# Optimization experiments

Measured on AMD Instinct MI355X. Metric: run time of the kernel, lower is better.

The kernel has to match this reference:

```python
import jax, jax.numpy as jnp
import numpy as np

B, D = 65536, 365

def _linp(k, fan_in, fan_out):
    # torch nn.Linear default init: U(-1/sqrt(fan_in), 1/sqrt(fan_in))
    kw, kb = jax.random.split(k)
    bound = 1.0 / np.sqrt(fan_in)
    W = jax.random.uniform(kw, (fan_in, fan_out), jnp.float32, -bound, bound)
    b = jax.random.uniform(kb, (fan_out,), jnp.float32, -bound, bound)
    return W, b

def setup_inputs() -> dict:
    key = jax.random.key(0)
    ks = jax.random.split(key, 9)
    x = jax.random.normal(ks[0], (B, D), jnp.float32)
    W1, b1 = _linp(ks[1], D, 512)
    W2, b2 = _linp(ks[2], 512, 256)
    W3, b3 = _linp(ks[3], 256, 128)
    Ws, bs = _linp(ks[4], 6, 32)
    Wc1, bc1 = _linp(ks[5], 128 + 32, 64)
    Wc2, bc2 = _linp(ks[6], 64, 32)
    Wc3, bc3 = _linp(ks[7], 32, 1)
    return dict(x=x, W1=W1, b1=b1, W2=W2, b2=b2, W3=W3, b3=b3,
                Ws=Ws, bs=bs, Wc1=Wc1, bc1=bc1, Wc2=Wc2, bc2=bc2,
                Wc3=Wc3, bc3=bc3)

def _row_stats(x):
    # fused row-wise moments: mean, std (ddof=1), min, max, skew, kurtosis
    mu = jnp.mean(x, axis=1, keepdims=True)          # [B,1]
    c = x - mu                                        # [B,D]
    var1 = jnp.sum(c * c, axis=1) / (x.shape[1] - 1)  # unbiased, matches torch.std()
    sigma = jnp.sqrt(var1)
    m3 = jnp.mean(c ** 3, axis=1)
    m4 = jnp.mean(c ** 4, axis=1)
    skew = m3 / (sigma ** 3 + 1e-8)
    kurt = m4 / (sigma ** 4 + 1e-8)
    return jnp.stack([mu[:, 0], sigma, jnp.min(x, axis=1), jnp.max(x, axis=1), skew, kurt], axis=1)

def reference(x, W1, b1, W2, b2, W3, b3, Ws, bs, Wc1, bc1, Wc2, bc2, Wc3, bc3):
    h = jax.nn.relu(x @ W1 + b1)
    h = jax.nn.relu(h @ W2 + b2)
    seq = jax.nn.relu(h @ W3 + b3)            # [B,128]
    stat = _row_stats(x) @ Ws + bs            # [B,32]
    comb = jnp.concatenate([seq, stat], axis=1)
    c = jax.nn.relu(comb @ Wc1 + bc1)
    c = jax.nn.relu(c @ Wc2 + bc2)
    out = jax.nn.sigmoid(c @ Wc3 + bc3)       # [B,1]
    return out[:, 0]
```

## Files before the change

### kernel.cpp

```cpp
#include <hip/hip_runtime.h>
#include <math.h>

typedef __attribute__((ext_vector_type(8)))  short short8;
typedef __attribute__((ext_vector_type(16))) float float16;
typedef __attribute__((ext_vector_type(4), aligned(4))) float float4a;

#define DEVI __device__ __forceinline__

DEVI short f2bf(float f) {
    unsigned u = __float_as_uint(f);
    u = (u + 0x7fffu + ((u >> 16) & 1u)) >> 16;
    return (short)u;
}
DEVI unsigned pk2(float a, float b) {
    return (unsigned)(unsigned short)f2bf(a) | ((unsigned)(unsigned short)f2bf(b) << 16);
}
DEVI float16 mfma16(short8 a, short8 b, float16 c) {
    return __builtin_amdgcn_mfma_f32_32x32x16_bf16(a, b, c, 0, 0, 0);
}
DEVI int rowof(int r, int h) { return (r & 3) + 8 * (r >> 2) + 4 * h; }
DEVI short8 lds8(const short* p) { return *(const short8*)p; }
DEVI short8 gld8(const short* p) { return *(const short8*)p; }

#define W1T_OFF  0
#define W2T_OFF  188416
#define W3T_OFF  319488
#define WC1T_OFF 352256
#define WC2T_OFF 362496

__global__ void prep_v2(const float* __restrict__ W1, const float* __restrict__ W2,
                        const float* __restrict__ W3, const float* __restrict__ Wc1,
                        const float* __restrict__ Wc2, short* __restrict__ ws) {
    __shared__ short T[16 * 72];
    int b = blockIdx.x, t = threadIdx.x;
    const float* src; int K, N; size_t base; int kc, nb;
    if (b < 184)        {            src = W1;  K = 365; N = 512; base = W1T_OFF;  kc = b >> 3;  nb = b & 7; }
    else if (b < 312)   { int l = b - 184; src = W2;  K = 512; N = 256; base = W2T_OFF;  kc = l >> 2;  nb = l & 3; }
    else if (b < 344)   { int l = b - 312; src = W3;  K = 256; N = 128; base = W3T_OFF;  kc = l >> 1;  nb = l & 1; }
    else if (b < 354)   {            src = Wc1; K = 160; N = 64;  base = WC1T_OFF; kc = b - 344; nb = 0; }
    else                {            src = Wc2; K = 64;  N = 32;  base = WC2T_OFF; kc = b - 354; nb = 0; }
    int n = nb * 64 + (t & 63);
    int kr = t >> 6;
    #pragma unroll
    for (int i = 0; i < 4; ++i) {
        int krow = kr + 4 * i;
        int k = kc * 16 + krow;
        float v = (k < K && n < N) ? src[(size_t)k * N + n] : 0.f;
        T[krow * 72 + (t & 63)] = f2bf(v);
    }
    __syncthreads();
    int n2 = t >> 2, ksq = (t & 3) * 4;
    int ng = nb * 64 + n2;
    if (ng < N) {
        unsigned lo = (unsigned)(unsigned short)T[ksq * 72 + n2]
                    | ((unsigned)(unsigned short)T[(ksq + 1) * 72 + n2] << 16);
        unsigned hi = (unsigned)(unsigned short)T[(ksq + 2) * 72 + n2]
                    | ((unsigned)(unsigned short)T[(ksq + 3) * 72 + n2] << 16);
        uint2 d; d.x = lo; d.y = hi;
        *(uint2*)(ws + base + ((size_t)kc * N + ng) * 16 + ksq) = d;
    }
}

__global__ __launch_bounds__(512, 4)
void fused_v7(const float* __restrict__ x,
              const float* __restrict__ b1f, const float* __restrict__ b2f,
              const float* __restrict__ b3f, const float* __restrict__ Wsf,
              const float* __restrict__ bsf, const float* __restrict__ bc1f,
              const float* __restrict__ bc2f, const float* __restrict__ Wc3f,
              const float* __restrict__ bc3f,
              const short* __restrict__ wsw, float* __restrict__ out)
{
    __shared__ __align__(16) char smem[70656];
    short* XT    = (short*)smem;
    short* SB    = (short*)(smem + 48128);
    short* FEATL = (short*)(smem + 65536);
    short* C1    = (short*)smem;
    float* C2    = (float*)(smem + 20480);

    const short* W1t  = wsw + W1T_OFF;
    const short* W2t  = wsw + W2T_OFF;
    const short* W3t  = wsw + W3T_OFF;
    const short* Wc1t = wsw + WC1T_OFF;
    const short* Wc2t = wsw + WC2T_OFF;

    const int tid  = (int)threadIdx.x;
    const int lane = tid & 63;
    const int wv   = tid >> 6;
    const int m    = lane & 31;
    const int h    = lane >> 5;
    const int rowBase = (int)blockIdx.x * 64;

    float bb1a = b1f[32 * wv + m];
    float bb1b = b1f[256 + 32 * wv + m];
    float bb2  = b2f[32 * wv + m];
    float bb3  = b3f[32 * (wv & 3) + m];

    const int rw = lane >> 3, q = lane & 7;
    const int xr = 8 * wv + rw;
    const float* xrow = x + (size_t)(rowBase + xr) * 365;
    float s1 = 0.f, s2 = 0.f, s3 = 0.f, s4 = 0.f, mn = 1e30f, mx = -1e30f;
    #pragma unroll
    for (int i = 0; i < 11; ++i) {
        float4a v = *(const float4a*)(xrow + 32 * i + 4 * q);
        #pragma unroll
        for (int j = 0; j < 4; ++j) {
            float f = v[j], f2 = f * f;
            s1 += f; s2 += f2; s3 += f2 * f; s4 += f2 * f2;
            mn = fminf(mn, f); mx = fmaxf(mx, f);
        }
        uint2 d; d.x = pk2(v[0], v[1]); d.y = pk2(v[2], v[3]);
        *(uint2*)(XT + xr * 376 + 32 * i + 4 * q) = d;
    }
    if (q < 3) {
        float4a v = *(const float4a*)(xrow + 352 + 4 * q);
        #pragma unroll
        for (int j = 0; j < 4; ++j) {
            float f = v[j], f2 = f * f;
            s1 += f; s2 += f2; s3 += f2 * f; s4 += f2 * f2;
            mn = fminf(mn, f); mx = fmaxf(mx, f);
        }
        uint2 d; d.x = pk2(v[0], v[1]); d.y = pk2(v[2], v[3]);
        *(uint2*)(XT + xr * 376 + 352 + 4 * q) = d;
    } else if (q == 3) {
        float f = xrow[364];
        float f2 = f * f;
        s1 += f; s2 += f2; s3 += f2 * f; s4 += f2 * f2;
        mn = fminf(mn, f); mx = fmaxf(mx, f);
        uint2 d; d.x = pk2(f, 0.f); d.y = 0u;
        *(uint2*)(XT + xr * 376 + 364) = d;
    }
    #pragma unroll
    for (int off = 1; off <= 4; off <<= 1) {
        s1 += __shfl_xor(s1, off); s2 += __shfl_xor(s2, off);
        s3 += __shfl_xor(s3, off); s4 += __shfl_xor(s4, off);
        mn = fminf(mn, __shfl_xor(mn, off)); mx = fmaxf(mx, __shfl_xor(mx, off));
    }
    {
        float mean  = s1 * (1.0f / 365.0f);
        float var1  = (s2 - 365.0f * mean * mean) * (1.0f / 364.0f);
        float sigma = sqrtf(var1);
        float m3 = (s3 - 3.0f * mean * s2) * (1.0f / 365.0f) + 2.0f * mean * mean * mean;
        float mm = mean * mean;
        float m4 = (s4 - 4.0f * mean * s3 + 6.0f * mm * s2) * (1.0f / 365.0f) - 3.0f * mm * mm;
        float sg2 = sigma * sigma;
        float skew = m3 / (sigma * sg2 + 1e-8f);
        float kurt = m4 / (sg2 * sg2 + 1e-8f);
        float st[6] = { mean, sigma, mn, mx, skew, kurt };
        float f[4];
        #pragma unroll
        for (int c0 = 0; c0 < 4; ++c0) {
            int c = 4 * q + c0;
            float acc = bsf[c];
            #pragma unroll
            for (int jj = 0; jj < 6; ++jj) acc += st[jj] * Wsf[jj * 32 + c];
            f[c0] = acc;
        }
        uint2 d; d.x = pk2(f[0], f[1]); d.y = pk2(f[2], f[3]);
        *(uint2*)(FEATL + xr * 40 + 4 * q) = d;
    }
    __syncthreads();

    float16 ha0, ha1;
    #pragma unroll
    for (int i = 0; i < 16; ++i) { ha0[i] = 0.f; ha1[i] = 0.f; }

    const short* Ap0  = XT + m * 376 + h * 8;
    const short* Ap1  = XT + (32 + m) * 376 + h * 8;
    const short* A2p0 = SB + m * 136 + h * 8;
    const short* A2p1 = SB + (32 + m) * 136 + h * 8;
    const int stcol = 32 * (wv & 3) + m;

    #pragma unroll
    for (int p = 0; p < 2; ++p) {
        float16 ga0, ga1;
        #pragma unroll
        for (int i = 0; i < 16; ++i) { ga0[i] = 0.f; ga1[i] = 0.f; }
        const short* B1 = W1t + (256 * p + 32 * wv + m) * 16 + h * 8;
        #pragma unroll
        for (int kc = 0; kc < 23; ++kc) {
            short8 b  = gld8(B1 + kc * 8192);
            short8 a0 = lds8(Ap0 + kc * 16);
            short8 a1 = lds8(Ap1 + kc * 16);
            ga0 = mfma16(a0, b, ga0);
            ga1 = mfma16(a1, b, ga1);
        }
        float bb = p ? bb1b : bb1a;
        #pragma unroll
        for (int s = 0; s < 2; ++s) {
            int sl = 2 * p + s;
            __syncthreads();
            if ((wv >> 2) == s) {
                #pragma unroll
                for (int r = 0; r < 16; ++r) {
                    SB[rowof(r, h) * 136 + stcol]        = f2bf(fmaxf(ga0[r] + bb, 0.f));
                    SB[(32 + rowof(r, h)) * 136 + stcol] = f2bf(fmaxf(ga1[r] + bb, 0.f));
                }
            }
            __syncthreads();
            const short* B2 = W2t + sl * 8 * 4096 + (32 * wv + m) * 16 + h * 8;
            #pragma unroll
            for (int i = 0; i < 8; ++i) {
                short8 b  = gld8(B2 + i * 4096);
                short8 a0 = lds8(A2p0 + i * 16);
                short8 a1 = lds8(A2p1 + i * 16);
                ha0 = mfma16(a0, b, ha0);
                ha1 = mfma16(a1, b, ha1);
            }
        }
    }

    float16 g3;
    #pragma unroll
    for (int i = 0; i < 16; ++i) g3[i] = 0.f;
    const short* A3p = SB + ((wv >> 2) * 32 + m) * 136 + h * 8;
    #pragma unroll
    for (int t = 0; t < 2; ++t) {
        __syncthreads();
        if ((wv >> 2) == t) {
            #pragma unroll
            for (int r = 0; r < 16; ++r) {
                SB[rowof(r, h) * 136 + stcol]        = f2bf(fmaxf(ha0[r] + bb2, 0.f));
                SB[(32 + rowof(r, h)) * 136 + stcol] = f2bf(fmaxf(ha1[r] + bb2, 0.f));
            }
        }
        __syncthreads();
        const short* B3 = W3t + t * 8 * 2048 + (32 * (wv & 3) + m) * 16 + h * 8;
        #pragma unroll
        for (int i = 0; i < 8; ++i) {
            short8 b = gld8(B3 + i * 2048);
            short8 a = lds8(A3p + i * 16);
            g3 = mfma16(a, b, g3);
        }
    }

    __syncthreads();
    {
        int rb = (wv >> 2) * 32;
        #pragma unroll
        for (int r = 0; r < 16; ++r)
            SB[(rb + rowof(r, h)) * 136 + stcol] = f2bf(fmaxf(g3[r] + bb3, 0.f));
    }
    __syncthreads();

    if (wv < 4) {
        int m4 = wv & 1, c4 = wv >> 1;
        const short* B4 = Wc1t + (32 * c4 + m) * 16 + h * 8;
        const short* A4 = SB + (m4 * 32 + m) * 136 + h * 8;
        float16 g4;
        #pragma unroll
        for (int i = 0; i < 16; ++i) g4[i] = 0.f;
        #pragma unroll
        for (int i = 0; i < 8; ++i) {
            short8 b = gld8(B4 + i * 1024);
            short8 a = lds8(A4 + i * 16);
            g4 = mfma16(a, b, g4);
        }
        const short* AF = FEATL + (m4 * 32 + m) * 40 + h * 8;
        #pragma unroll
        for (int i = 0; i < 2; ++i) {
            short8 b = gld8(B4 + (8 + i) * 1024);
            short8 a = lds8(AF + i * 16);
            g4 = mfma16(a, b, g4);
        }
        float bb = bc1f[32 * c4 + m];
        #pragma unroll
        for (int r = 0; r < 16; ++r)
            C1[(m4 * 32 + rowof(r, h)) * 72 + 32 * c4 + m] = f2bf(fmaxf(g4[r] + bb, 0.f));
    }
    __syncthreads();

    if (wv < 2) {
        const short* B5 = Wc2t + m * 16 + h * 8;
        const short* A5 = C1 + (wv * 32 + m) * 72 + h * 8;
        float16 g5;
        #pragma unroll
        for (int i = 0; i < 16; ++i) g5[i] = 0.f;
        #pragma unroll
        for (int i = 0; i < 4; ++i) {
            short8 b = gld8(B5 + i * 512);
            short8 a = lds8(A5 + i * 16);
            g5 = mfma16(a, b, g5);
        }
        float bb = bc2f[m];
        #pragma unroll
        for (int r = 0; r < 16; ++r)
            C2[(wv * 32 + rowof(r, h)) * 33 + m] = fmaxf(g5[r] + bb, 0.f);
    }
    __syncthreads();

    if (tid < 64) {
        float z = bc3f[0];
        #pragma unroll
        for (int i = 0; i < 32; ++i) z += C2[tid * 33 + i] * Wc3f[i];
        out[rowBase + tid] = 1.0f / (1.0f + expf(-z));
    }
}

extern "C" void kernel_launch(void* const* d_in, const int* in_sizes, int n_in,
                              void* d_out, int out_size, void* d_ws, size_t ws_size,
                              hipStream_t stream)
{
    (void)in_sizes; (void)n_in; (void)out_size; (void)ws_size;
    const float* x   = (const float*)d_in[0];
    const float* W1  = (const float*)d_in[1];
    const float* b1  = (const float*)d_in[2];
    const float* W2  = (const float*)d_in[3];
    const float* b2  = (const float*)d_in[4];
    const float* W3  = (const float*)d_in[5];
    const float* b3  = (const float*)d_in[6];
    const float* Ws  = (const float*)d_in[7];
    const float* bs  = (const float*)d_in[8];
    const float* Wc1 = (const float*)d_in[9];
    const float* bc1 = (const float*)d_in[10];
    const float* Wc2 = (const float*)d_in[11];
    const float* bc2 = (const float*)d_in[12];
    const float* Wc3 = (const float*)d_in[13];
    const float* bc3 = (const float*)d_in[14];
    short* ws = (short*)d_ws;

    prep_v2<<<358, 256, 0, stream>>>(W1, W2, W3, Wc1, Wc2, ws);
    fused_v7<<<1024, 512, 0, stream>>>(x, b1, b2, b3, Ws, bs, bc1, bc2, Wc3, bc3,
                                       ws, (float*)d_out);
}
```

Baseline: 218.7 us.

## Widen LDS staging buffer to cut barrier rounds and spill stat features to global

```diff
diff --git a/kernel.cpp b/kernel.cpp
--- a/kernel.cpp
+++ b/kernel.cpp
@@ -27,6 +27,7 @@
 #define W3T_OFF  319488
 #define WC1T_OFF 352256
 #define WC2T_OFF 362496
+#define FEATG_OFF 364544ull
 
 __global__ void prep_v2(const float* __restrict__ W1, const float* __restrict__ W2,
                         const float* __restrict__ W3, const float* __restrict__ Wc1,
@@ -62,26 +63,27 @@
 }
 
 __global__ __launch_bounds__(512, 4)
-void fused_v7(const float* __restrict__ x,
+void fused_v8(const float* __restrict__ x,
               const float* __restrict__ b1f, const float* __restrict__ b2f,
               const float* __restrict__ b3f, const float* __restrict__ Wsf,
               const float* __restrict__ bsf, const float* __restrict__ bc1f,
               const float* __restrict__ bc2f, const float* __restrict__ Wc3f,
               const float* __restrict__ bc3f,
-              const short* __restrict__ wsw, float* __restrict__ out)
+              short* __restrict__ wsw, float* __restrict__ out)
 {
-    __shared__ __align__(16) char smem[70656];
-    short* XT    = (short*)smem;
-    short* SB    = (short*)(smem + 48128);
-    short* FEATL = (short*)(smem + 65536);
-    short* C1    = (short*)smem;
-    float* C2    = (float*)(smem + 20480);
+    __shared__ __align__(16) char smem[81920];
+    short* XT  = (short*)smem;
+    short* SB  = (short*)(smem + 48640);
+    short* SEQ = (short*)smem;
+    short* C1  = (short*)(smem + 17408);
+    float* C2  = (float*)(smem + 26624);
 
     const short* W1t  = wsw + W1T_OFF;
     const short* W2t  = wsw + W2T_OFF;
     const short* W3t  = wsw + W3T_OFF;
     const short* Wc1t = wsw + WC1T_OFF;
     const short* Wc2t = wsw + WC2T_OFF;
+    short* featg      = wsw + FEATG_OFF;
 
     const int tid  = (int)threadIdx.x;
     const int lane = tid & 63;
@@ -109,7 +111,7 @@
             mn = fminf(mn, f); mx = fmaxf(mx, f);
         }
         uint2 d; d.x = pk2(v[0], v[1]); d.y = pk2(v[2], v[3]);
-        *(uint2*)(XT + xr * 376 + 32 * i + 4 * q) = d;
+        *(uint2*)(XT + xr * 380 + 32 * i + 4 * q) = d;
     }
     if (q < 3) {
         float4a v = *(const float4a*)(xrow + 352 + 4 * q);
@@ -120,14 +122,14 @@
             mn = fminf(mn, f); mx = fmaxf(mx, f);
         }
         uint2 d; d.x = pk2(v[0], v[1]); d.y = pk2(v[2], v[3]);
-        *(uint2*)(XT + xr * 376 + 352 + 4 * q) = d;
+        *(uint2*)(XT + xr * 380 + 352 + 4 * q) = d;
     } else if (q == 3) {
         float f = xrow[364];
         float f2 = f * f;
         s1 += f; s2 += f2; s3 += f2 * f; s4 += f2 * f2;
         mn = fminf(mn, f); mx = fmaxf(mx, f);
         uint2 d; d.x = pk2(f, 0.f); d.y = 0u;
-        *(uint2*)(XT + xr * 376 + 364) = d;
+        *(uint2*)(XT + xr * 380 + 364) = d;
     }
     #pragma unroll
     for (int off = 1; off <= 4; off <<= 1) {
@@ -156,7 +158,7 @@
             f[c0] = acc;
         }
         uint2 d; d.x = pk2(f[0], f[1]); d.y = pk2(f[2], f[3]);
-        *(uint2*)(FEATL + xr * 40 + 4 * q) = d;
+        *(uint2*)(featg + (size_t)(rowBase + xr) * 32 + 4 * q) = d;
     }
     __syncthreads();
 
@@ -164,11 +166,11 @@
     #pragma unroll
     for (int i = 0; i < 16; ++i) { ha0[i] = 0.f; ha1[i] = 0.f; }
 
-    const short* Ap0  = XT + m * 376 + h * 8;
-    const short* Ap1  = XT + (32 + m) * 376 + h * 8;
-    const short* A2p0 = SB + m * 136 + h * 8;
-    const short* A2p1 = SB + (32 + m) * 136 + h * 8;
-    const int stcol = 32 * (wv & 3) + m;
+    const short* Ap0  = XT + m * 380 + h * 8;
+    const short* Ap1  = XT + (32 + m) * 380 + h * 8;
+    const short* A2p0 = SB + m * 260 + h * 8;
+    const short* A2p1 = SB + (32 + m) * 260 + h * 8;
+    const int stcol = 32 * wv + m;
 
     #pragma unroll
     for (int p = 0; p < 2; ++p) {
@@ -185,67 +187,55 @@
             ga1 = mfma16(a1, b, ga1);
         }
         float bb = p ? bb1b : bb1a;
-        #pragma unroll
-        for (int s = 0; s < 2; ++s) {
-            int sl = 2 * p + s;
-            __syncthreads();
-            if ((wv >> 2) == s) {
-                #pragma unroll
-                for (int r = 0; r < 16; ++r) {
-                    SB[rowof(r, h) * 136 + stcol]        = f2bf(fmaxf(ga0[r] + bb, 0.f));
-                    SB[(32 + rowof(r, h)) * 136 + stcol] = f2bf(fmaxf(ga1[r] + bb, 0.f));
-                }
-            }
-            __syncthreads();
-            const short* B2 = W2t + sl * 8 * 4096 + (32 * wv + m) * 16 + h * 8;
-            #pragma unroll
-            for (int i = 0; i < 8; ++i) {
-                short8 b  = gld8(B2 + i * 4096);
-                short8 a0 = lds8(A2p0 + i * 16);
-                short8 a1 = lds8(A2p1 + i * 16);
-                ha0 = mfma16(a0, b, ha0);
-                ha1 = mfma16(a1, b, ha1);
-            }
-        }
-    }
-
+        if (p) __syncthreads();
+        #pragma unroll
+        for (int r = 0; r < 16; ++r) {
+            int rr = rowof(r, h);
+            SB[rr * 260 + stcol]        = f2bf(fmaxf(ga0[r] + bb, 0.f));
+            SB[(32 + rr) * 260 + stcol] = f2bf(fmaxf(ga1[r] + bb, 0.f));
+        }
+        __syncthreads();
+        const short* B2 = W2t + p * 16 * 4096 + (32 * wv + m) * 16 + h * 8;
+        #pragma unroll
+        for (int i = 0; i < 16; ++i) {
+            short8 b  = gld8(B2 + i * 4096);
+            short8 a0 = lds8(A2p0 + i * 16);
+            short8 a1 = lds8(A2p1 + i * 16);
+            ha0 = mfma16(a0, b, ha0);
+            ha1 = mfma16(a1, b, ha1);
+        }
+    }
+
+    __syncthreads();
+    #pragma unroll
+    for (int r = 0; r < 16; ++r) {
+        int rr = rowof(r, h);
+        SB[rr * 260 + stcol]        = f2bf(fmaxf(ha0[r] + bb2, 0.f));
+        SB[(32 + rr) * 260 + stcol] = f2bf(fmaxf(ha1[r] + bb2, 0.f));
+    }
+    __syncthreads();
+
+    const int cg3 = wv & 3, rh3 = wv >> 2;
     float16 g3;
     #pragma unroll
     for (int i = 0; i < 16; ++i) g3[i] = 0.f;
-    const short* A3p = SB + ((wv >> 2) * 32 + m) * 136 + h * 8;
-    #pragma unroll
-    for (int t = 0; t < 2; ++t) {
-        __syncthreads();
-        if ((wv >> 2) == t) {
-            #pragma unroll
-            for (int r = 0; r < 16; ++r) {
-                SB[rowof(r, h) * 136 + stcol]        = f2bf(fmaxf(ha0[r] + bb2, 0.f));
-                SB[(32 + rowof(r, h)) * 136 + stcol] = f2bf(fmaxf(ha1[r] + bb2, 0.f));
-            }
-        }
-        __syncthreads();
-        const short* B3 = W3t + t * 8 * 2048 + (32 * (wv & 3) + m) * 16 + h * 8;
-        #pragma unroll
-        for (int i = 0; i < 8; ++i) {
-            short8 b = gld8(B3 + i * 2048);
-            short8 a = lds8(A3p + i * 16);
-            g3 = mfma16(a, b, g3);
-        }
-    }
-
-    __syncthreads();
-    {
-        int rb = (wv >> 2) * 32;
-        #pragma unroll
-        for (int r = 0; r < 16; ++r)
-            SB[(rb + rowof(r, h)) * 136 + stcol] = f2bf(fmaxf(g3[r] + bb3, 0.f));
-    }
+    const short* A3 = SB + (32 * rh3 + m) * 260 + h * 8;
+    const short* B3 = W3t + (32 * cg3 + m) * 16 + h * 8;
+    #pragma unroll
+    for (int i = 0; i < 16; ++i) {
+        short8 b = gld8(B3 + i * 2048);
+        short8 a = lds8(A3 + i * 16);
+        g3 = mfma16(a, b, g3);
+    }
+    #pragma unroll
+    for (int r = 0; r < 16; ++r)
+        SEQ[(32 * rh3 + rowof(r, h)) * 136 + 32 * cg3 + m] = f2bf(fmaxf(g3[r] + bb3, 0.f));
     __syncthreads();
 
     if (wv < 4) {
         int m4 = wv & 1, c4 = wv >> 1;
         const short* B4 = Wc1t + (32 * c4 + m) * 16 + h * 8;
-        const short* A4 = SB + (m4 * 32 + m) * 136 + h * 8;
+        const short* A4 = SEQ + (32 * m4 + m) * 136 + h * 8;
         float16 g4;
         #pragma unroll
         for (int i = 0; i < 16; ++i) g4[i] = 0.f;
@@ -255,17 +245,13 @@
             short8 a = lds8(A4 + i * 16);
             g4 = mfma16(a, b, g4);
         }
-        const short* AF = FEATL + (m4 * 32 + m) * 40 + h * 8;
-        #pragma unroll
-        for (int i = 0; i < 2; ++i) {
-            short8 b = gld8(B4 + (8 + i) * 1024);
-            short8 a = lds8(AF + i * 16);
-            g4 = mfma16(a, b, g4);
-        }
+        const short* AF = featg + (size_t)(rowBase + 32 * m4 + m) * 32 + h * 8;
+        g4 = mfma16(gld8(AF),      gld8(B4 + 8 * 1024), g4);
+        g4 = mfma16(gld8(AF + 16), gld8(B4 + 9 * 1024), g4);
         float bb = bc1f[32 * c4 + m];
         #pragma unroll
         for (int r = 0; r < 16; ++r)
-            C1[(m4 * 32 + rowof(r, h)) * 72 + 32 * c4 + m] = f2bf(fmaxf(g4[r] + bb, 0.f));
+            C1[(32 * m4 + rowof(r, h)) * 72 + 32 * c4 + m] = f2bf(fmaxf(g4[r] + bb, 0.f));
     }
     __syncthreads();
 
@@ -319,6 +305,6 @@
     short* ws = (short*)d_ws;
 
     prep_v2<<<358, 256, 0, stream>>>(W1, W2, W3, Wc1, Wc2, ws);
-    fused_v7<<<1024, 512, 0, stream>>>(x, b1, b2, b3, Ws, bs, bc1, bc2, Wc3, bc3,
+    fused_v8<<<1024, 512, 0, stream>>>(x, b1, b2, b3, Ws, bs, bc1, bc2, Wc3, bc3,
                                        ws, (float*)d_out);
 }
```

Measured after the change: 318.9 us. +45.8%, slower.
